# Kernel tuning notes

Hardware: AMD Instinct MI355X
Metric: run time of the kernel (lower is better)

The kernel has to match this reference:

```python
import jax, jax.numpy as jnp
import numpy as np

NUM_EMB = 512
DIM = 65        # so dim-1 = 64 Householder reflections of size 64x64 per embedding
B, N = 2048, 256


def setup_inputs() -> dict:
    key = jax.random.key(0)
    k1, k2, k3, k4 = jax.random.split(key, 4)
    x = jax.random.normal(k1, (B, N, DIM), dtype=jnp.float32)
    r_idx = jax.random.randint(k2, (B,), 0, NUM_EMB)
    # learned params: embedding table and scalar flip_sign (nn.Parameter)
    emb_weight = jax.random.normal(k3, (NUM_EMB, (DIM - 1) * (DIM - 1)), dtype=jnp.float32)
    flip_sign = jax.random.normal(k4, (), dtype=jnp.float32)
    return {"x": x, "r_idx": r_idx, "emb_weight": emb_weight, "flip_sign": flip_sign}


def _flg_forward(x, emb_weight, flip_sign, r_idx):
    d = DIM - 1
    # GELU (exact, matching torch default) then view as [E, d, d]; row w is a reflection vector v
    v = jax.nn.gelu(emb_weight, approximate=False).reshape(NUM_EMB, d, d)
    # Householder matrices H[e, w] = I - 2 v v^T / (v . v)   -> [E, d, d, d]
    outer = jnp.einsum('ewv,ewk->ewvk', v, v)
    sqnorm = jnp.einsum('ewv,ewv->ew', v, v)[..., None, None]
    H = jnp.eye(d, dtype=x.dtype) - 2.0 * outer / sqnorm
    H = jnp.transpose(H, (1, 0, 2, 3))  # [d, E, d, d]: reflection index leading (scan axis)

    # sequential product W = I @ H[0] @ H[1] @ ... @ H[d-1], batched over E
    W0 = jnp.broadcast_to(jnp.eye(d, dtype=x.dtype), (NUM_EMB, d, d))
    def step(carry, Hi):
        return carry @ Hi, None
    W, _ = jax.lax.scan(step, W0, H)  # [E, d, d]

    # scale last column by flip_sign (in-place mul in torch)
    W = W.at[:, :, -1].multiply(flip_sign)

    Wb = W[r_idx]                        # [B, d, d]
    x0 = x[..., :1]                      # [B, N, 1]
    xn = jnp.einsum('bnd,bdc->bnc', x[..., 1:], Wb)  # rotate remaining coords
    return jnp.concatenate([x0, xn], axis=-1)


def reference(x, r_idx, emb_weight, flip_sign):
    xo = _flg_forward(x, emb_weight, flip_sign, r_idx)
    return (xo, r_idx)
```

## Files before the change

### kernel.cpp

```cpp
#include <hip/hip_runtime.h>
#include <math.h>

#define NUM_EMB 512
#define DIMV 65
#define DD   64
#define BB   2048
#define NN   256

typedef short short8 __attribute__((ext_vector_type(8)));
typedef float f32x4  __attribute__((ext_vector_type(4)));

__device__ __forceinline__ float gelu_exact(float x) {
    return 0.5f * x * (1.0f + erff(x * 0.7071067811865475f));
}

__device__ __forceinline__ unsigned f2bf_u(float f) {
    unsigned u = __builtin_bit_cast(unsigned, f);
    u += 0x7FFFu + ((u >> 16) & 1u);
    return u >> 16;
}
__device__ __forceinline__ unsigned short f2bf(float f) {
    return (unsigned short)f2bf_u(f);
}

__global__ __launch_bounds__(256) void build_W(const float* __restrict__ emb,
                                               const float* __restrict__ flip_sign,
                                               const int*   __restrict__ r_idx,
                                               unsigned short* __restrict__ WgT,
                                               float* __restrict__ out) {
    __shared__ float v_lds[DD * DD];
    __shared__ float s_lds[DD];
    const int e = blockIdx.x;
    const int t = threadIdx.x;
    const int r = t >> 2;
    const int q = t & 3;

    const float* erow = emb + (size_t)e * (DD * DD);
    #pragma unroll
    for (int p = 0; p < 16; ++p) {
        int idx = p * 256 + t;
        v_lds[idx] = gelu_exact(erow[idx]);
    }

    if (t < 4) {
        int bi = e * 4 + t;
        out[(size_t)BB * NN * DIMV + bi] = (float)r_idx[bi];
    }
    __syncthreads();

    {
        const float* vr = &v_lds[r * DD + q * 16];
        float ss = 0.f;
        #pragma unroll
        for (int k = 0; k < 16; ++k) ss += vr[k] * vr[k];
        ss += __shfl_xor(ss, 1);
        ss += __shfl_xor(ss, 2);
        if (q == 0) s_lds[r] = 2.0f / ss;
    }
    __syncthreads();

    float Wq[16];
    #pragma unroll
    for (int k = 0; k < 16; ++k) Wq[k] = ((q * 16 + k) == r) ? 1.0f : 0.0f;

    float vv[16], nv[16];
    {
        const float* vr = &v_lds[q * 16];
        *(float4*)&nv[0]  = *(const float4*)&vr[0];
        *(float4*)&nv[4]  = *(const float4*)&vr[4];
        *(float4*)&nv[8]  = *(const float4*)&vr[8];
        *(float4*)&nv[12] = *(const float4*)&vr[12];
    }

    for (int w = 0; w < DD; ++w) {
        #pragma unroll
        for (int k = 0; k < 16; ++k) vv[k] = nv[k];
        if (w < DD - 1) {
            const float* vr = &v_lds[(w + 1) * DD + q * 16];
            *(float4*)&nv[0]  = *(const float4*)&vr[0];
            *(float4*)&nv[4]  = *(const float4*)&vr[4];
            *(float4*)&nv[8]  = *(const float4*)&vr[8];
            *(float4*)&nv[12] = *(const float4*)&vr[12];
        }
        float p0 = Wq[0] * vv[0],  p1 = Wq[1] * vv[1];
        float p2 = Wq[2] * vv[2],  p3 = Wq[3] * vv[3];
        #pragma unroll
        for (int k = 4; k < 16; k += 4) {
            p0 += Wq[k]     * vv[k];
            p1 += Wq[k + 1] * vv[k + 1];
            p2 += Wq[k + 2] * vv[k + 2];
            p3 += Wq[k + 3] * vv[k + 3];
        }
        float p = (p0 + p1) + (p2 + p3);
        p += __shfl_xor(p, 1);
        p += __shfl_xor(p, 2);
        const float sc = s_lds[w] * p;
        #pragma unroll
        for (int k = 0; k < 16; ++k) Wq[k] -= sc * vv[k];
    }

    if (q == 3) Wq[15] *= flip_sign[0];

    unsigned short* wd = WgT + (size_t)e * (DD * DD) + r;
    #pragma unroll
    for (int k = 0; k < 16; ++k)
        wd[(16 * q + k) * DD] = f2bf(Wq[k]);
}

__global__ __launch_bounds__(256) void apply_W(const float* __restrict__ x,
                                               const int*   __restrict__ r_idx,
                                               const unsigned short* __restrict__ WgT,
                                               float* __restrict__ out) {
    __shared__ alignas(16) float X[128 * DIMV];
    const int blk  = blockIdx.x;
    const int b    = blk >> 1;
    const int half = blk & 1;
    const size_t rowbase = (size_t)b * NN + half * 128;
    const int t = threadIdx.x;

    const int e = r_idx[b];

    const int w     = t >> 6;
    const int l     = t & 63;
    const int lrow  = l & 15;
    const int kslot = l >> 4;
    const int r0    = w * 32;

    const unsigned short* wb = WgT + (size_t)e * (DD * DD);
    short8 bfrg[4][2];
    #pragma unroll
    for (int ct = 0; ct < 4; ++ct)
        #pragma unroll
        for (int kb = 0; kb < 2; ++kb)
            bfrg[ct][kb] = *(const short8*)(wb + (ct * 16 + lrow) * DD + kb * 32 + kslot * 8);

    {
        const float4* xs = (const float4*)(x + rowbase * DIMV);
        float4* Xv = (float4*)X;
        float4 v[8];
        #pragma unroll
        for (int p = 0; p < 8; ++p) v[p] = xs[p * 256 + t];
        float4 vt;
        if (t < 32) vt = xs[2048 + t];
        #pragma unroll
        for (int p = 0; p < 8; ++p) Xv[p * 256 + t] = v[p];
        if (t < 32) Xv[2048 + t] = vt;
    }
    __syncthreads();

    short8 afrg[2][2];
    #pragma unroll
    for (int rt = 0; rt < 2; ++rt)
        #pragma unroll
        for (int kb = 0; kb < 2; ++kb) {
            const float* xp = &X[(r0 + rt * 16 + lrow) * DIMV + 1 + kb * 32 + kslot * 8];
            union { short8 s; unsigned u[4]; } af;
            #pragma unroll
            for (int j = 0; j < 4; ++j)
                af.u[j] = f2bf_u(xp[2 * j]) | (f2bf_u(xp[2 * j + 1]) << 16);
            afrg[rt][kb] = af.s;
        }

    f32x4 acc[2][4];
    #pragma unroll
    for (int rt = 0; rt < 2; ++rt)
        #pragma unroll
        for (int ct = 0; ct < 4; ++ct) {
            f32x4 c0 = {0.f, 0.f, 0.f, 0.f};
            c0 = __builtin_amdgcn_mfma_f32_16x16x32_bf16(afrg[rt][0], bfrg[ct][0], c0, 0, 0, 0);
            c0 = __builtin_amdgcn_mfma_f32_16x16x32_bf16(afrg[rt][1], bfrg[ct][1], c0, 0, 0, 0);
            acc[rt][ct] = c0;
        }

    #pragma unroll
    for (int rt = 0; rt < 2; ++rt)
        #pragma unroll
        for (int ct = 0; ct < 4; ++ct)
            #pragma unroll
            for (int rg = 0; rg < 4; ++rg)
                X[(r0 + rt * 16 + kslot * 4 + rg) * DIMV + 1 + ct * 16 + lrow] = acc[rt][ct][rg];
    __syncthreads();

    {
        float4* og = (float4*)(out + rowbase * DIMV);
        const float4* Xv = (const float4*)X;
        #pragma unroll
        for (int p = 0; p < 8; ++p) og[p * 256 + t] = Xv[p * 256 + t];
        if (t < 32) og[2048 + t] = Xv[2048 + t];
    }
}

extern "C" void kernel_launch(void* const* d_in, const int* in_sizes, int n_in,
                              void* d_out, int out_size, void* d_ws, size_t ws_size,
                              hipStream_t stream) {
    const float* x         = (const float*)d_in[0];
    const int*   r_idx     = (const int*)d_in[1];
    const float* emb       = (const float*)d_in[2];
    const float* flip_sign = (const float*)d_in[3];
    float* out = (float*)d_out;
    unsigned short* WgT = (unsigned short*)d_ws;

    build_W<<<NUM_EMB, 256, 0, stream>>>(emb, flip_sign, r_idx, WgT, out);
    apply_W<<<BB * 2, 256, 0, stream>>>(x, r_idx, WgT, out);
}
```

Baseline: 77.13 us.

## Make apply_W persistent over 8 tiles with double-buffered global prefetch

apply_W now has each block handle eight 64-row tiles (two batch entries) instead of one 128-row half-batch. It prefetches the next tile's x into registers while the current tile is converted, multiplied and written back. Two LDS buffers alternate between tiles, and W fragments are reloaded only when the batch entry changes. The aim is to hide global load latency and cut the number of launched blocks. In exchange the grid shrinks to 1024 blocks, which may reduce occupancy and latency hiding across CUs, and each tile now needs two barriers.

```diff
diff --git a/kernel.cpp b/kernel.cpp
--- a/kernel.cpp
+++ b/kernel.cpp
@@ -6,6 +6,10 @@
 #define DD   64
 #define BB   2048
 #define NN   256
+#define TPB  8
+#define GRID_APPLY ((BB * NN) / (64 * TPB))
+#define TFLOATS (64 * DIMV)
+#define TVEC4   (TFLOATS / 4)
 
 typedef short short8 __attribute__((ext_vector_type(8)));
 typedef float f32x4  __attribute__((ext_vector_type(4)));
@@ -111,82 +115,106 @@
                                                const int*   __restrict__ r_idx,
                                                const unsigned short* __restrict__ WgT,
                                                float* __restrict__ out) {
-    __shared__ alignas(16) float X[128 * DIMV];
-    const int blk  = blockIdx.x;
-    const int b    = blk >> 1;
-    const int half = blk & 1;
-    const size_t rowbase = (size_t)b * NN + half * 128;
+    __shared__ alignas(16) float X[2][TFLOATS];
     const int t = threadIdx.x;
-
-    const int e = r_idx[b];
-
-    const int w     = t >> 6;
-    const int l     = t & 63;
+    const int w = t >> 6;
+    const int l = t & 63;
     const int lrow  = l & 15;
     const int kslot = l >> 4;
-    const int r0    = w * 32;
-
-    const unsigned short* wb = WgT + (size_t)e * (DD * DD);
+    const int r0    = w * 16;
+
+    const int tile0 = blockIdx.x * TPB;
+    const int b0    = tile0 >> 2;
+
+    int e0 = r_idx[b0];
+    int e1 = r_idx[b0 + 1];
+
+    float4 v[2][4];
+    float4 vt[2];
     short8 bfrg[4][2];
-    #pragma unroll
-    for (int ct = 0; ct < 4; ++ct)
-        #pragma unroll
-        for (int kb = 0; kb < 2; ++kb)
-            bfrg[ct][kb] = *(const short8*)(wb + (ct * 16 + lrow) * DD + kb * 32 + kslot * 8);
-
-    {
-        const float4* xs = (const float4*)(x + rowbase * DIMV);
-        float4* Xv = (float4*)X;
-        float4 v[8];
-        #pragma unroll
-        for (int p = 0; p < 8; ++p) v[p] = xs[p * 256 + t];
-        float4 vt;
-        if (t < 32) vt = xs[2048 + t];
-        #pragma unroll
-        for (int p = 0; p < 8; ++p) Xv[p * 256 + t] = v[p];
-        if (t < 32) Xv[2048 + t] = vt;
-    }
-    __syncthreads();
-
-    short8 afrg[2][2];
-    #pragma unroll
-    for (int rt = 0; rt < 2; ++rt)
+
+    {
+        const float4* xs = (const float4*)(x + (size_t)tile0 * TFLOATS);
+        #pragma unroll
+        for (int p = 0; p < 4; ++p) v[0][p] = xs[p * 256 + t];
+        if (t < 16) vt[0] = xs[1024 + t];
+    }
+    {
+        const unsigned short* wb = WgT + (size_t)e0 * (DD * DD);
+        #pragma unroll
+        for (int ct = 0; ct < 4; ++ct)
+            #pragma unroll
+            for (int kb = 0; kb < 2; ++kb)
+                bfrg[ct][kb] = *(const short8*)(wb + (ct * 16 + lrow) * DD + kb * 32 + kslot * 8);
+    }
+
+    #pragma unroll
+    for (int i = 0; i < TPB; ++i) {
+        const int J = i & 1;
+
+        if (i + 1 < TPB) {
+            const float4* xs = (const float4*)(x + (size_t)(tile0 + i + 1) * TFLOATS);
+            #pragma unroll
+            for (int p = 0; p < 4; ++p) v[J ^ 1][p] = xs[p * 256 + t];
+            if (t < 16) vt[J ^ 1] = xs[1024 + t];
+        }
+        if (i == 4) {
+            const unsigned short* wb = WgT + (size_t)e1 * (DD * DD);
+            #pragma unroll
+            for (int ct = 0; ct < 4; ++ct)
+                #pragma unroll
+                for (int kb = 0; kb < 2; ++kb)
+                    bfrg[ct][kb] = *(const short8*)(wb + (ct * 16 + lrow) * DD + kb * 32 + kslot * 8);
+        }
+
+        {
+            float4* Xv = (float4*)X[J];
+            #pragma unroll
+            for (int p = 0; p < 4; ++p) Xv[p * 256 + t] = v[J][p];
+            if (t < 16) Xv[1024 + t] = vt[J];
+        }
+
+        asm volatile("s_waitcnt lgkmcnt(0)" ::: "memory");
+        __builtin_amdgcn_s_barrier();
+        __builtin_amdgcn_sched_barrier(0);
+
+        short8 afrg[2];
         #pragma unroll
         for (int kb = 0; kb < 2; ++kb) {
-            const float* xp = &X[(r0 + rt * 16 + lrow) * DIMV + 1 + kb * 32 + kslot * 8];
+            const float* xp = &X[J][(r0 + lrow) * DIMV + 1 + kb * 32 + kslot * 8];
             union { short8 s; unsigned u[4]; } af;
             #pragma unroll
-            for (int j = 0; j < 4; ++j)
-                af.u[j] = f2bf_u(xp[2 * j]) | (f2bf_u(xp[2 * j + 1]) << 16);
-            afrg[rt][kb] = af.s;
-        }
-
-    f32x4 acc[2][4];
-    #pragma unroll
-    for (int rt = 0; rt < 2; ++rt)
+            for (int jj = 0; jj < 4; ++jj)
+                af.u[jj] = f2bf_u(xp[2 * jj]) | (f2bf_u(xp[2 * jj + 1]) << 16);
+            afrg[kb] = af.s;
+        }
+
+        f32x4 acc[4];
         #pragma unroll
         for (int ct = 0; ct < 4; ++ct) {
             f32x4 c0 = {0.f, 0.f, 0.f, 0.f};
-            c0 = __builtin_amdgcn_mfma_f32_16x16x32_bf16(afrg[rt][0], bfrg[ct][0], c0, 0, 0, 0);
-            c0 = __builtin_amdgcn_mfma_f32_16x16x32_bf16(afrg[rt][1], bfrg[ct][1], c0, 0, 0, 0);
-            acc[rt][ct] = c0;
-        }
-
-    #pragma unroll
-    for (int rt = 0; rt < 2; ++rt)
+            c0 = __builtin_amdgcn_mfma_f32_16x16x32_bf16(afrg[0], bfrg[ct][0], c0, 0, 0, 0);
+            c0 = __builtin_amdgcn_mfma_f32_16x16x32_bf16(afrg[1], bfrg[ct][1], c0, 0, 0, 0);
+            acc[ct] = c0;
+        }
+
         #pragma unroll
         for (int ct = 0; ct < 4; ++ct)
             #pragma unroll
             for (int rg = 0; rg < 4; ++rg)
-                X[(r0 + rt * 16 + kslot * 4 + rg) * DIMV + 1 + ct * 16 + lrow] = acc[rt][ct][rg];
-    __syncthreads();
-
-    {
-        float4* og = (float4*)(out + rowbase * DIMV);
-        const float4* Xv = (const float4*)X;
-        #pragma unroll
-        for (int p = 0; p < 8; ++p) og[p * 256 + t] = Xv[p * 256 + t];
-        if (t < 32) og[2048 + t] = Xv[2048 + t];
+                X[J][(r0 + kslot * 4 + rg) * DIMV + 1 + ct * 16 + lrow] = acc[ct][rg];
+
+        asm volatile("s_waitcnt lgkmcnt(0)" ::: "memory");
+        __builtin_amdgcn_s_barrier();
+        __builtin_amdgcn_sched_barrier(0);
+
+        {
+            float4* og = (float4*)(out + (size_t)(tile0 + i) * TFLOATS);
+            const float4* Xv = (const float4*)X[J];
+            #pragma unroll
+            for (int p = 0; p < 4; ++p) og[p * 256 + t] = Xv[p * 256 + t];
+            if (t < 16) og[1024 + t] = Xv[1024 + t];
+        }
     }
 }
 
@@ -201,5 +229,5 @@
     unsigned short* WgT = (unsigned short*)d_ws;
 
     build_W<<<NUM_EMB, 256, 0, stream>>>(emb, flip_sign, r_idx, WgT, out);
-    apply_W<<<BB * 2, 256, 0, stream>>>(x, r_idx, WgT, out);
-}
+    apply_W<<<GRID_APPLY, 256, 0, stream>>>(x, r_idx, WgT, out);
+}
```

After: 81.03 us. +5.0%, slower.

## Load x directly into registers per wave and stream output through per-wave LDS tiles

Applied to the files above, without the earlier changes.

apply_W no longer stages the whole 128-row x tile in shared memory behind block-wide barriers. Each wave now loads its 64 rows straight from global memory into registers with unaligned vector loads, converts them to bf16, and writes each 16-row result tile through a small per-wave LDS image before a coalesced store, using only an lgkmcnt wait. The grid is halved so each block covers one batch element. This removes __syncthreads and the big LDS footprint, which should help occupancy and overlap. The cost is strided, unaligned global reads of x and an implicit reliance on in-order execution within a wave for LDS reuse.

```diff
diff --git a/kernel.cpp b/kernel.cpp
--- a/kernel.cpp
+++ b/kernel.cpp
@@ -6,9 +6,11 @@
 #define DD   64
 #define BB   2048
 #define NN   256
+#define IMGF (16 * DIMV)
 
 typedef short short8 __attribute__((ext_vector_type(8)));
 typedef float f32x4  __attribute__((ext_vector_type(4)));
+typedef float f4u    __attribute__((ext_vector_type(4), aligned(4)));
 
 __device__ __forceinline__ float gelu_exact(float x) {
     return 0.5f * x * (1.0f + erff(x * 0.7071067811865475f));
@@ -111,20 +113,19 @@
                                                const int*   __restrict__ r_idx,
                                                const unsigned short* __restrict__ WgT,
                                                float* __restrict__ out) {
-    __shared__ alignas(16) float X[128 * DIMV];
-    const int blk  = blockIdx.x;
-    const int b    = blk >> 1;
-    const int half = blk & 1;
-    const size_t rowbase = (size_t)b * NN + half * 128;
+    __shared__ alignas(16) float IMG[4][IMGF];
     const int t = threadIdx.x;
-
-    const int e = r_idx[b];
-
-    const int w     = t >> 6;
-    const int l     = t & 63;
+    const int w = t >> 6;
+    const int l = t & 63;
     const int lrow  = l & 15;
     const int kslot = l >> 4;
-    const int r0    = w * 32;
+
+    const int gw = blockIdx.x * 4 + w;
+    const size_t row0 = (size_t)gw * 64;
+    const int b = gw >> 2;
+
+    const int e = r_idx[b];
+    float* img = IMG[w];
 
     const unsigned short* wb = WgT + (size_t)e * (DD * DD);
     short8 bfrg[4][2];
@@ -134,59 +135,60 @@
         for (int kb = 0; kb < 2; ++kb)
             bfrg[ct][kb] = *(const short8*)(wb + (ct * 16 + lrow) * DD + kb * 32 + kslot * 8);
 
-    {
-        const float4* xs = (const float4*)(x + rowbase * DIMV);
-        float4* Xv = (float4*)X;
-        float4 v[8];
-        #pragma unroll
-        for (int p = 0; p < 8; ++p) v[p] = xs[p * 256 + t];
-        float4 vt;
-        if (t < 32) vt = xs[2048 + t];
-        #pragma unroll
-        for (int p = 0; p < 8; ++p) Xv[p * 256 + t] = v[p];
-        if (t < 32) Xv[2048 + t] = vt;
-    }
-    __syncthreads();
-
-    short8 afrg[2][2];
-    #pragma unroll
-    for (int rt = 0; rt < 2; ++rt)
+    f4u   av[4][4];
+    float x0v[4];
+    #pragma unroll
+    for (int i = 0; i < 4; ++i) {
+        const float* xr = x + (row0 + i * 16 + lrow) * DIMV + 1 + kslot * 8;
+        av[i][0] = *(const f4u*)(xr);
+        av[i][1] = *(const f4u*)(xr + 4);
+        av[i][2] = *(const f4u*)(xr + 32);
+        av[i][3] = *(const f4u*)(xr + 36);
+        x0v[i] = (l < 16) ? x[(row0 + i * 16 + l) * DIMV] : 0.f;
+    }
+    __builtin_amdgcn_sched_barrier(0);
+
+    #pragma unroll
+    for (int i = 0; i < 4; ++i) {
+        short8 afrg[2];
         #pragma unroll
         for (int kb = 0; kb < 2; ++kb) {
-            const float* xp = &X[(r0 + rt * 16 + lrow) * DIMV + 1 + kb * 32 + kslot * 8];
             union { short8 s; unsigned u[4]; } af;
-            #pragma unroll
-            for (int j = 0; j < 4; ++j)
-                af.u[j] = f2bf_u(xp[2 * j]) | (f2bf_u(xp[2 * j + 1]) << 16);
-            afrg[rt][kb] = af.s;
-        }
-
-    f32x4 acc[2][4];
-    #pragma unroll
-    for (int rt = 0; rt < 2; ++rt)
+            const f4u a0 = av[i][kb * 2 + 0];
+            const f4u a1 = av[i][kb * 2 + 1];
+            af.u[0] = f2bf_u(a0.x) | (f2bf_u(a0.y) << 16);
+            af.u[1] = f2bf_u(a0.z) | (f2bf_u(a0.w) << 16);
+            af.u[2] = f2bf_u(a1.x) | (f2bf_u(a1.y) << 16);
+            af.u[3] = f2bf_u(a1.z) | (f2bf_u(a1.w) << 16);
+            afrg[kb] = af.s;
+        }
+
+        f32x4 acc[4];
         #pragma unroll
         for (int ct = 0; ct < 4; ++ct) {
             f32x4 c0 = {0.f, 0.f, 0.f, 0.f};
-            c0 = __builtin_amdgcn_mfma_f32_16x16x32_bf16(afrg[rt][0], bfrg[ct][0], c0, 0, 0, 0);
-            c0 = __builtin_amdgcn_mfma_f32_16x16x32_bf16(afrg[rt][1], bfrg[ct][1], c0, 0, 0, 0);
-            acc[rt][ct] = c0;
-        }
-
-    #pragma unroll
-    for (int rt = 0; rt < 2; ++rt)
+            c0 = __builtin_amdgcn_mfma_f32_16x16x32_bf16(afrg[0], bfrg[ct][0], c0, 0, 0, 0);
+            c0 = __builtin_amdgcn_mfma_f32_16x16x32_bf16(afrg[1], bfrg[ct][1], c0, 0, 0, 0);
+            acc[ct] = c0;
+        }
+
         #pragma unroll
         for (int ct = 0; ct < 4; ++ct)
             #pragma unroll
             for (int rg = 0; rg < 4; ++rg)
-                X[(r0 + rt * 16 + kslot * 4 + rg) * DIMV + 1 + ct * 16 + lrow] = acc[rt][ct][rg];
-    __syncthreads();
-
-    {
-        float4* og = (float4*)(out + rowbase * DIMV);
-        const float4* Xv = (const float4*)X;
-        #pragma unroll
-        for (int p = 0; p < 8; ++p) og[p * 256 + t] = Xv[p * 256 + t];
-        if (t < 32) og[2048 + t] = Xv[2048 + t];
+                img[(kslot * 4 + rg) * DIMV + 1 + ct * 16 + lrow] = acc[ct][rg];
+        if (l < 16) img[l * DIMV] = x0v[i];
+
+        asm volatile("s_waitcnt lgkmcnt(0)" ::: "memory");
+        __builtin_amdgcn_sched_barrier(0);
+
+        {
+            float4* og = (float4*)(out + (row0 + i * 16) * DIMV);
+            const float4* iv = (const float4*)img;
+            #pragma unroll
+            for (int p = 0; p < 4; ++p) og[p * 64 + l] = iv[p * 64 + l];
+            if (l < 4) og[256 + l] = iv[256 + l];
+        }
     }
 }
 
@@ -201,5 +203,5 @@
     unsigned short* WgT = (unsigned short*)d_ws;
 
     build_W<<<NUM_EMB, 256, 0, stream>>>(emb, flip_sign, r_idx, WgT, out);
-    apply_W<<<BB * 2, 256, 0, stream>>>(x, r_idx, WgT, out);
-}
+    apply_W<<<BB, 256, 0, stream>>>(x, r_idx, WgT, out);
+}
```

New measurement: 79.54 us. +3.1%, slower.
